# Optimization experiments

Hardware: AMD Instinct MI355X
Metric: run time of the kernel (lower is better)

## Reference

```python
import jax, jax.numpy as jnp
import numpy as np

B, N, L, E, U, G, R, D, C = 64, 50000, 8, 100000, 20000, 20000, 64, 16, 2


def setup_inputs() -> dict:
    rng = np.random.default_rng(0)
    key = jax.random.key(0)
    ks = jax.random.split(key, 10)
    # index structures (duplicate-free where the torch code assumes uniqueness)
    gene_map = jnp.asarray(rng.choice(N, G, replace=False).astype(np.int32))
    dst_unique = jnp.stack([jnp.asarray(rng.choice(N, U, replace=False).astype(np.int32)) for _ in range(L)])
    root_ids = jnp.asarray(rng.choice(N, R, replace=False).astype(np.int32))
    src = jax.random.randint(ks[0], (L, E), 0, N, dtype=jnp.int32)
    dst_pos = jax.random.randint(ks[1], (L, E), 0, U, dtype=jnp.int32)
    # data and parameters
    X_gene_batch = jax.random.normal(ks[2], (B, G), jnp.float32)
    w_in = jax.random.normal(ks[3], (D,), jnp.float32) * 0.5   # Linear(1, d) weight
    b_in = jax.random.normal(ks[4], (D,), jnp.float32) * 0.1
    W = jax.random.normal(ks[5], (L, D, D), jnp.float32) * (1.0 / np.sqrt(D))  # xavier-ish
    bias = jnp.zeros((N, D), jnp.float32)
    W_head = jax.random.normal(ks[6], (C, R * D), jnp.float32) * (1.0 / np.sqrt(R * D))
    b_head = jnp.zeros((C,), jnp.float32)
    return {
        "X_gene_batch": X_gene_batch, "w_in": w_in, "b_in": b_in, "W": W,
        "bias": bias, "W_head": W_head, "b_head": b_head,
        "gene_map": gene_map, "src": src, "dst_pos": dst_pos,
        "dst_unique": dst_unique, "root_ids": root_ids,
    }


def reference(X_gene_batch, w_in, b_in, W, bias, W_head, b_head,
              gene_map, src, dst_pos, dst_unique, root_ids):
    Bn = X_gene_batch.shape[0]
    n_nodes, d = bias.shape
    n_layers = W.shape[0]
    u = dst_unique.shape[1]
    # _init_state_vector: h=0, scatter in_proj(X[...,None]) at gene_map
    gene_emb = X_gene_batch[..., None] * w_in + b_in          # [B, G, d]
    h = jnp.zeros((Bn, n_nodes, d), X_gene_batch.dtype)
    h = h.at[:, gene_map].set(gene_emb)
    for li in range(n_layers):
        h_src = h[:, src[li]]                                  # gather [B, E, d]
        msg = jnp.einsum('bed,df->bef', h_src, W[li])          # small dxd matmul
        agg = jnp.zeros((Bn, u, d), h.dtype).at[:, dst_pos[li]].add(msg)  # scatter-add
        h_dst = jnp.tanh(agg + bias[dst_unique[li]][None])     # bias lookup + tanh (dropout=0)
        h = h.at[:, dst_unique[li]].set(h_dst)                 # write back
    feat = h[:, root_ids].reshape(Bn, -1)                      # roots_concat readout
    return feat @ W_head.T + b_head                            # [B, C]
```

## Files before the change

### kernel.cpp

```cpp
#include <hip/hip_runtime.h>
#include <hip/hip_fp16.h>
#include <cmath>

constexpr int B_ = 64, N_ = 50000, L_ = 8, E_ = 100000, U_ = 20000, G_ = 20000, R_ = 64, D_ = 16, C_ = 2;
constexpr int EPL_ = E_ + 3 * U_ + 8;
constexpr int BC = 64;
constexpr int F = BC * 2;


__device__ __forceinline__ float tanh_fast(float x) {
  float e = __expf(2.0f * x);
  return 1.0f - 2.0f * __builtin_amdgcn_rcpf(e + 1.0f);
}


__global__ __launch_bounds__(256) void hist_kernel(
    const int* __restrict__ dst_pos, int* __restrict__ cnt,
    int* __restrict__ rank) {
  int e = blockIdx.x * 256 + threadIdx.x;
  int li = blockIdx.y;
  if (e >= E_) return;
  rank[li * E_ + e] = atomicAdd(&cnt[li * U_ + dst_pos[li * E_ + e]], 1);
}

__global__ __launch_bounds__(1024) void scan_kernel(
    const int* __restrict__ cnt, int* __restrict__ offs) {
  __shared__ int sums[1024];
  int li = blockIdx.x, t = threadIdx.x;
  int base = t * 20;
  int v[20];
  int s = 0;
#pragma unroll
  for (int i = 0; i < 20; ++i) {
    int idx = base + i;
    int c = (idx < U_) ? cnt[li * U_ + idx] : 0;
    v[i] = s;
    s += (c + 3) & ~3;
  }
  sums[t] = s;
  __syncthreads();
  for (int off = 1; off < 1024; off <<= 1) {
    int o = (t >= off) ? sums[t - off] : 0;
    __syncthreads();
    sums[t] += o;
    __syncthreads();
  }
  int excl = sums[t] - s;
#pragma unroll
  for (int i = 0; i < 20; ++i) {
    int idx = base + i;
    if (idx < U_) offs[li * (U_ + 1) + idx] = excl + v[i];
  }
  if (t == 1023) offs[li * (U_ + 1) + U_] = sums[1023];
}

__global__ __launch_bounds__(256) void scatter_kernel(
    const int* __restrict__ dst_pos, const int* __restrict__ src,
    const int* __restrict__ offs, const int* __restrict__ rank,
    int* __restrict__ ssrc) {
  int e = blockIdx.x * 256 + threadIdx.x;
  int li = blockIdx.y;
  if (e >= E_) return;
  int u = dst_pos[li * E_ + e];
  int p = offs[li * (U_ + 1) + u] + rank[li * E_ + e];
  ssrc[(size_t)li * EPL_ + p] = src[li * E_ + e];
}

__global__ __launch_bounds__(256) void pad_fill_k(
    const int* __restrict__ cnt, const int* __restrict__ offs,
    int* __restrict__ ssrc) {
  int t = blockIdx.x * 256 + threadIdx.x;
  if (t >= L_ * U_) return;
  int li = t / U_, u = t % U_;
  int end = offs[li * (U_ + 1) + u] + cnt[li * U_ + u];
  int pend = offs[li * (U_ + 1) + u + 1];
  int* sp = ssrc + (size_t)li * EPL_;
  for (int p = end; p < pend; ++p) sp[p] = N_;
  if (u == U_ - 1) {
    int ptot = offs[li * (U_ + 1) + U_];
    for (int p = ptot; p < ptot + 8; ++p) sp[p] = N_;
  }
}


__global__ __launch_bounds__(256) void gene_init_k(
    const float* __restrict__ X, const float* __restrict__ w_in,
    const float* __restrict__ b_in, const int* __restrict__ gene_map,
    float4* __restrict__ h4) {
  int t = blockIdx.x * 256 + threadIdx.x;
  if (t >= G_ * BC) return;
  int b = t % BC;
  int g = t / BC;
  float x = X[b * G_ + g];
  int node = gene_map[g];
  float4 out[2];
  __half2* oh = reinterpret_cast<__half2*>(out);
#pragma unroll
  for (int k = 0; k < 8; ++k) {
    float r0 = fmaf(x, w_in[2 * k], b_in[2 * k]);
    float r1 = fmaf(x, w_in[2 * k + 1], b_in[2 * k + 1]);
    oh[k] = __float22half2_rn(make_float2(r0, r1));
  }
  h4[(size_t)node * F + b * 2] = out[0];
  h4[(size_t)node * F + b * 2 + 1] = out[1];
}

__global__ __launch_bounds__(256) void gather_k(
    const float4* __restrict__ h4, const int* __restrict__ offs,
    const int* __restrict__ ssrc, float4* __restrict__ agg4, int li) {
  int tid = threadIdx.x;
  int wave = tid >> 6, lane = tid & 63;
  int w = blockIdx.x * 4 + wave;
  int u0 = w * 4;
  const int* ob = offs + li * (U_ + 1) + u0;
  int offv[5];
#pragma unroll
  for (int i = 0; i < 5; ++i) offv[i] = ob[i];
  const int* sp = ssrc + (size_t)li * EPL_;

  __half2 acc[2][2][4];
  const __half2 z = __half2half2(__float2half(0.f));
#pragma unroll
  for (int j = 0; j < 2; ++j)
#pragma unroll
    for (int r = 0; r < 2; ++r)
#pragma unroll
      for (int k = 0; k < 4; ++k) acc[j][r][k] = z;

  auto flushu = [&](int u) {
#pragma unroll
    for (int r = 0; r < 2; ++r) {
      float4 outv;
      __half2* ov = reinterpret_cast<__half2*>(&outv);
#pragma unroll
      for (int k = 0; k < 4; ++k) {
        float2 f0 = __half22float2(acc[0][r][k]);
        float2 f1 = __half22float2(acc[1][r][k]);
        ov[k] = __float22half2_rn(make_float2(f0.x + f1.x, f0.y + f1.y));
      }
      agg4[(size_t)u * F + lane + r * 64] = outv;
    }
#pragma unroll
    for (int j = 0; j < 2; ++j)
#pragma unroll
      for (int r = 0; r < 2; ++r)
#pragma unroll
        for (int k = 0; k < 4; ++k) acc[j][r][k] = z;
  };

  auto loadRows = [&](float4 (&v)[4][2], int4 id) {
    v[0][0] = h4[(size_t)id.x * F + lane]; v[0][1] = h4[(size_t)id.x * F + lane + 64];
    v[1][0] = h4[(size_t)id.y * F + lane]; v[1][1] = h4[(size_t)id.y * F + lane + 64];
    v[2][0] = h4[(size_t)id.z * F + lane]; v[2][1] = h4[(size_t)id.z * F + lane + 64];
    v[3][0] = h4[(size_t)id.w * F + lane]; v[3][1] = h4[(size_t)id.w * F + lane + 64];
  };
  auto accum = [&](const float4 (&v)[4][2]) {
#pragma unroll
    for (int j = 0; j < 4; ++j)
#pragma unroll
      for (int r = 0; r < 2; ++r) {
        const __half2* p = reinterpret_cast<const __half2*>(&v[j][r]);
#pragma unroll
        for (int k = 0; k < 4; ++k)
          acc[j & 1][r][k] = __hadd2(acc[j & 1][r][k], p[k]);
      }
  };

  int e = offv[0];
  int eend = offv[4];
  int uj = 0;
  while (uj < 4 && offv[uj + 1] == e) { flushu(u0 + uj); ++uj; }
  if (e >= eend) return;

  float4 va[4][2], vb[4][2];
  int4 idC = *(const int4*)(sp + e);
  int4 idN = *(const int4*)(sp + e + 4);
  loadRows(va, idC);

  for (;;) {
    loadRows(vb, idN);
    idN = *(const int4*)(sp + e + 8);
    accum(va);
    e += 4;
    if (e == offv[uj + 1]) {
      flushu(u0 + uj); ++uj;
      while (uj < 4 && offv[uj + 1] == e) { flushu(u0 + uj); ++uj; }
    }
    if (e >= eend) break;
    loadRows(va, idN);
    idN = *(const int4*)(sp + e + 8);
    accum(vb);
    e += 4;
    if (e == offv[uj + 1]) {
      flushu(u0 + uj); ++uj;
      while (uj < 4 && offv[uj + 1] == e) { flushu(u0 + uj); ++uj; }
    }
    if (e >= eend) break;
  }
}

__global__ __launch_bounds__(256) void dense_k(
    const float4* __restrict__ agg4, const float* __restrict__ W,
    const float* __restrict__ bias, const int* __restrict__ dst_unique,
    float4* __restrict__ h4, int li) {
  __shared__ float Wlds[256];
  int tid = threadIdx.x;
  Wlds[tid] = W[li * 256 + tid];
  __syncthreads();
  int t = blockIdx.x * 256 + tid;
  int u = t >> 6, b = t & 63;
  float4 c0 = agg4[(size_t)u * F + b * 2];
  float4 c1 = agg4[(size_t)u * F + b * 2 + 1];
  float a[16];
  {
    const __half2* p0 = reinterpret_cast<const __half2*>(&c0);
    const __half2* p1 = reinterpret_cast<const __half2*>(&c1);
#pragma unroll
    for (int k = 0; k < 4; ++k) {
      float2 f0 = __half22float2(p0[k]);
      float2 f1 = __half22float2(p1[k]);
      a[2 * k] = f0.x; a[2 * k + 1] = f0.y;
      a[8 + 2 * k] = f1.x; a[8 + 2 * k + 1] = f1.y;
    }
  }
  float m[16];
#pragma unroll
  for (int j = 0; j < 16; ++j) m[j] = 0.f;
#pragma unroll
  for (int d = 0; d < 16; ++d) {
    float s = a[d];
    const float4* wr = (const float4*)&Wlds[d * 16];
    float4 w0 = wr[0], w1 = wr[1], w2 = wr[2], w3 = wr[3];
    m[0] = fmaf(s, w0.x, m[0]);  m[1] = fmaf(s, w0.y, m[1]);
    m[2] = fmaf(s, w0.z, m[2]);  m[3] = fmaf(s, w0.w, m[3]);
    m[4] = fmaf(s, w1.x, m[4]);  m[5] = fmaf(s, w1.y, m[5]);
    m[6] = fmaf(s, w1.z, m[6]);  m[7] = fmaf(s, w1.w, m[7]);
    m[8] = fmaf(s, w2.x, m[8]);  m[9] = fmaf(s, w2.y, m[9]);
    m[10] = fmaf(s, w2.z, m[10]); m[11] = fmaf(s, w2.w, m[11]);
    m[12] = fmaf(s, w3.x, m[12]); m[13] = fmaf(s, w3.y, m[13]);
    m[14] = fmaf(s, w3.z, m[14]); m[15] = fmaf(s, w3.w, m[15]);
  }
  int node = dst_unique[li * U_ + u];
  const float4* bp = (const float4*)(bias + (size_t)node * 16);
  float4 b0 = bp[0], b1 = bp[1], b2 = bp[2], b3 = bp[3];
  float bb[16] = {b0.x, b0.y, b0.z, b0.w, b1.x, b1.y, b1.z, b1.w,
                  b2.x, b2.y, b2.z, b2.w, b3.x, b3.y, b3.z, b3.w};
  float4 o0, o1;
  __half2* ov0 = reinterpret_cast<__half2*>(&o0);
  __half2* ov1 = reinterpret_cast<__half2*>(&o1);
#pragma unroll
  for (int k = 0; k < 4; ++k) {
    ov0[k] = __float22half2_rn(make_float2(tanh_fast(m[2 * k] + bb[2 * k]),
                                           tanh_fast(m[2 * k + 1] + bb[2 * k + 1])));
    ov1[k] = __float22half2_rn(make_float2(tanh_fast(m[8 + 2 * k] + bb[8 + 2 * k]),
                                           tanh_fast(m[8 + 2 * k + 1] + bb[8 + 2 * k + 1])));
  }
  h4[(size_t)node * F + b * 2] = o0;
  h4[(size_t)node * F + b * 2 + 1] = o1;
}

__global__ __launch_bounds__(64) void head_k(
    const float4* __restrict__ h4, const float* __restrict__ W_head,
    const float* __restrict__ b_head, const int* __restrict__ root_ids,
    float* __restrict__ out) {
  int bl = blockIdx.x;
  int r = threadIdx.x;
  int node = root_ids[r];
  float4 p0 = h4[(size_t)node * F + bl * 2];
  float4 p1 = h4[(size_t)node * F + bl * 2 + 1];
  float v[16];
  const __half2* ph0 = reinterpret_cast<const __half2*>(&p0);
  const __half2* ph1 = reinterpret_cast<const __half2*>(&p1);
#pragma unroll
  for (int k = 0; k < 4; ++k) {
    float2 f0 = __half22float2(ph0[k]);
    float2 f1 = __half22float2(ph1[k]);
    v[2 * k] = f0.x; v[2 * k + 1] = f0.y;
    v[8 + 2 * k] = f1.x; v[8 + 2 * k + 1] = f1.y;
  }
  float acc0 = 0.f, acc1 = 0.f;
#pragma unroll
  for (int d = 0; d < 16; ++d) {
    acc0 = fmaf(v[d], W_head[r * 16 + d], acc0);
    acc1 = fmaf(v[d], W_head[1024 + r * 16 + d], acc1);
  }
  for (int off = 32; off; off >>= 1) {
    acc0 += __shfl_down(acc0, off, 64);
    acc1 += __shfl_down(acc1, off, 64);
  }
  if (r == 0) {
    out[bl * 2 + 0] = acc0 + b_head[0];
    out[bl * 2 + 1] = acc1 + b_head[1];
  }
}

__global__ void zero_out_k(float* out, int n) {
  int t = blockIdx.x * 256 + threadIdx.x;
  if (t < n) out[t] = 0.f;
}


static size_t need_bytes() {
  return (size_t)(N_ + 1) * F * 16 + (size_t)U_ * F * 16 +
         (size_t)L_ * U_ * 4 +
         (size_t)L_ * (U_ + 1) * 4 +
         (size_t)L_ * E_ * 4 +
         (size_t)L_ * EPL_ * 4;
}

extern "C" void kernel_launch(void* const* d_in, const int* in_sizes, int n_in,
                              void* d_out, int out_size, void* d_ws, size_t ws_size,
                              hipStream_t stream) {
  if (ws_size < need_bytes()) {
    zero_out_k<<<(out_size + 255) / 256, 256, 0, stream>>>((float*)d_out, out_size);
    return;
  }
  const float* X = (const float*)d_in[0];
  const float* w_in = (const float*)d_in[1];
  const float* b_in = (const float*)d_in[2];
  const float* W = (const float*)d_in[3];
  const float* bias = (const float*)d_in[4];
  const float* W_head = (const float*)d_in[5];
  const float* b_head = (const float*)d_in[6];
  const int* gene_map = (const int*)d_in[7];
  const int* src = (const int*)d_in[8];
  const int* dst_pos = (const int*)d_in[9];
  const int* dst_unique = (const int*)d_in[10];
  const int* root_ids = (const int*)d_in[11];
  float* out = (float*)d_out;

  const size_t h_bytes = (size_t)(N_ + 1) * F * 16;
  const size_t agg_bytes = (size_t)U_ * F * 16;
  const size_t cnt_bytes = (size_t)L_ * U_ * 4;
  const size_t offs_bytes = (size_t)L_ * (U_ + 1) * 4;
  const size_t rank_bytes = (size_t)L_ * E_ * 4;

  char* ws = (char*)d_ws;
  float4* h4 = (float4*)ws;
  float4* agg4 = (float4*)(ws + h_bytes);
  int* cnt = (int*)(ws + h_bytes + agg_bytes);
  int* offs = (int*)(ws + h_bytes + agg_bytes + cnt_bytes);
  int* rank = (int*)(ws + h_bytes + agg_bytes + cnt_bytes + offs_bytes);
  int* ssrc = (int*)(ws + h_bytes + agg_bytes + cnt_bytes + offs_bytes + rank_bytes);

  hipMemsetAsync(cnt, 0, cnt_bytes, stream);
  hipMemsetAsync(h4, 0, h_bytes, stream);
  dim3 egrid((E_ + 255) / 256, L_);
  hist_kernel<<<egrid, 256, 0, stream>>>(dst_pos, cnt, rank);
  scan_kernel<<<L_, 1024, 0, stream>>>(cnt, offs);
  scatter_kernel<<<egrid, 256, 0, stream>>>(dst_pos, src, offs, rank, ssrc);
  pad_fill_k<<<(L_ * U_ + 255) / 256, 256, 0, stream>>>(cnt, offs, ssrc);

  gene_init_k<<<(G_ * BC + 255) / 256, 256, 0, stream>>>(X, w_in, b_in, gene_map, h4);

  const int gather_grid = U_ / 16;
  const int dense_grid = U_ * BC / 256;
  for (int li = 0; li < L_; ++li) {
    gather_k<<<gather_grid, 256, 0, stream>>>(h4, offs, ssrc, agg4, li);
    dense_k<<<dense_grid, 256, 0, stream>>>(agg4, W, bias, dst_unique, h4, li);
  }

  head_k<<<BC, 64, 0, stream>>>(h4, W_head, b_head, root_ids, out);
}
```

Before: 669.5 us.

## Balance gather work by assigning fixed edge-group chunks per wave instead of fixed nodes

```diff
diff --git a/kernel.cpp b/kernel.cpp
--- a/kernel.cpp
+++ b/kernel.cpp
@@ -3,7 +3,9 @@
 #include <cmath>
 
 constexpr int B_ = 64, N_ = 50000, L_ = 8, E_ = 100000, U_ = 20000, G_ = 20000, R_ = 64, D_ = 16, C_ = 2;
-constexpr int EPL_ = E_ + 3 * U_ + 8;
+constexpr int EPL_ = E_ + 3 * U_ + 4096;
+constexpr int EPLG_ = EPL_ / 4 + 16;
+constexpr int GPW = 8;
 constexpr int BC = 64;
 constexpr int F = BC * 2;
 
@@ -33,9 +35,10 @@
 #pragma unroll
   for (int i = 0; i < 20; ++i) {
     int idx = base + i;
-    int c = (idx < U_) ? cnt[li * U_ + idx] : 0;
+    int c = (idx < U_) ? cnt[li * U_ + idx] : -1;
+    int pc = (c < 0) ? 0 : ((c == 0) ? 4 : ((c + 3) & ~3));
     v[i] = s;
-    s += (c + 3) & ~3;
+    s += pc;
   }
   sums[t] = s;
   __syncthreads();
@@ -66,16 +69,19 @@
   ssrc[(size_t)li * EPL_ + p] = src[li * E_ + e];
 }
 
-__global__ __launch_bounds__(256) void pad_fill_k(
+__global__ __launch_bounds__(256) void pad_fill_ug_k(
     const int* __restrict__ cnt, const int* __restrict__ offs,
-    int* __restrict__ ssrc) {
+    int* __restrict__ ssrc, int* __restrict__ ug) {
   int t = blockIdx.x * 256 + threadIdx.x;
   if (t >= L_ * U_) return;
   int li = t / U_, u = t % U_;
-  int end = offs[li * (U_ + 1) + u] + cnt[li * U_ + u];
+  int start = offs[li * (U_ + 1) + u];
+  int end = start + cnt[li * U_ + u];
   int pend = offs[li * (U_ + 1) + u + 1];
   int* sp = ssrc + (size_t)li * EPL_;
   for (int p = end; p < pend; ++p) sp[p] = N_;
+  int* ugp = ug + (size_t)li * EPLG_;
+  for (int g = start >> 2; g < (pend >> 2); ++g) ugp[g] = u;
   if (u == U_ - 1) {
     int ptot = offs[li * (U_ + 1) + U_];
     for (int p = ptot; p < ptot + 8; ++p) sp[p] = N_;
@@ -106,17 +112,21 @@
 }
 
 __global__ __launch_bounds__(256) void gather_k(
-    const float4* __restrict__ h4, const int* __restrict__ offs,
+    const float4* __restrict__ h4, const int* __restrict__ ug,
     const int* __restrict__ ssrc, float4* __restrict__ agg4, int li) {
   int tid = threadIdx.x;
   int wave = tid >> 6, lane = tid & 63;
-  int w = blockIdx.x * 4 + wave;
-  int u0 = w * 4;
-  const int* ob = offs + li * (U_ + 1) + u0;
-  int offv[5];
-#pragma unroll
-  for (int i = 0; i < 5; ++i) offv[i] = ob[i];
+  int wv = blockIdx.x * 4 + wave;
+  int g0 = wv * GPW, gend = g0 + GPW;
+  const int* ugp = ug + (size_t)li * EPLG_;
   const int* sp = ssrc + (size_t)li * EPL_;
+
+  int prevU = (g0 == 0) ? -2 : ugp[g0 - 1];
+  int g = g0;
+  while (g < gend && ugp[g] == prevU) ++g;
+  if (g >= gend) return;
+  int curU = ugp[g];
+  if (curU < 0) return;
 
   __half2 acc[2][2][4];
   const __half2 z = __half2half2(__float2half(0.f));
@@ -166,36 +176,43 @@
       }
   };
 
-  int e = offv[0];
-  int eend = offv[4];
-  int uj = 0;
-  while (uj < 4 && offv[uj + 1] == e) { flushu(u0 + uj); ++uj; }
-  if (e >= eend) return;
-
   float4 va[4][2], vb[4][2];
-  int4 idC = *(const int4*)(sp + e);
-  int4 idN = *(const int4*)(sp + e + 4);
-  loadRows(va, idC);
+  int4 idA = *(const int4*)(sp + 4 * g);
+  loadRows(va, idA);
+  int nuA = ugp[g + 1];
+  int nuB;
 
   for (;;) {
-    loadRows(vb, idN);
-    idN = *(const int4*)(sp + e + 8);
-    accum(va);
-    e += 4;
-    if (e == offv[uj + 1]) {
-      flushu(u0 + uj); ++uj;
-      while (uj < 4 && offv[uj + 1] == e) { flushu(u0 + uj); ++uj; }
+    {
+      bool more = (nuA >= 0) && ((nuA == curU) || (g + 1 < gend));
+      if (more) {
+        int4 idB = *(const int4*)(sp + 4 * (g + 1));
+        loadRows(vb, idB);
+        nuB = ugp[g + 2];
+      }
+      accum(va);
+      if (nuA != curU) {
+        flushu(curU);
+        if (!more) return;
+        curU = nuA;
+      }
+      ++g;
     }
-    if (e >= eend) break;
-    loadRows(va, idN);
-    idN = *(const int4*)(sp + e + 8);
-    accum(vb);
-    e += 4;
-    if (e == offv[uj + 1]) {
-      flushu(u0 + uj); ++uj;
-      while (uj < 4 && offv[uj + 1] == e) { flushu(u0 + uj); ++uj; }
+    {
+      bool more = (nuB >= 0) && ((nuB == curU) || (g + 1 < gend));
+      if (more) {
+        int4 idA2 = *(const int4*)(sp + 4 * (g + 1));
+        loadRows(va, idA2);
+        nuA = ugp[g + 2];
+      }
+      accum(vb);
+      if (nuB != curU) {
+        flushu(curU);
+        if (!more) return;
+        curU = nuB;
+      }
+      ++g;
     }
-    if (e >= eend) break;
   }
 }
 
@@ -334,6 +351,7 @@
   const size_t cnt_bytes = (size_t)L_ * U_ * 4;
   const size_t offs_bytes = (size_t)L_ * (U_ + 1) * 4;
   const size_t rank_bytes = (size_t)L_ * E_ * 4;
+  const size_t ug_bytes = (size_t)L_ * EPLG_ * 4;
 
   char* ws = (char*)d_ws;
   float4* h4 = (float4*)ws;
@@ -341,7 +359,9 @@
   int* cnt = (int*)(ws + h_bytes + agg_bytes);
   int* offs = (int*)(ws + h_bytes + agg_bytes + cnt_bytes);
   int* rank = (int*)(ws + h_bytes + agg_bytes + cnt_bytes + offs_bytes);
+  int* ug = rank;
   int* ssrc = (int*)(ws + h_bytes + agg_bytes + cnt_bytes + offs_bytes + rank_bytes);
+  (void)ug_bytes;
 
   hipMemsetAsync(cnt, 0, cnt_bytes, stream);
   hipMemsetAsync(h4, 0, h_bytes, stream);
@@ -349,14 +369,17 @@
   hist_kernel<<<egrid, 256, 0, stream>>>(dst_pos, cnt, rank);
   scan_kernel<<<L_, 1024, 0, stream>>>(cnt, offs);
   scatter_kernel<<<egrid, 256, 0, stream>>>(dst_pos, src, offs, rank, ssrc);
-  pad_fill_k<<<(L_ * U_ + 255) / 256, 256, 0, stream>>>(cnt, offs, ssrc);
+  hipMemsetAsync(ug, 0xFF, ug_bytes, stream);
+  pad_fill_ug_k<<<(L_ * U_ + 255) / 256, 256, 0, stream>>>(cnt, offs, ssrc, ug);
 
   gene_init_k<<<(G_ * BC + 255) / 256, 256, 0, stream>>>(X, w_in, b_in, gene_map, h4);
 
-  const int gather_grid = U_ / 16;
+  const int total_groups = EPL_ / 4;
+  const int gwaves = (total_groups + GPW - 1) / GPW;
+  const int gather_grid = (gwaves + 3) / 4;
   const int dense_grid = U_ * BC / 256;
   for (int li = 0; li < L_; ++li) {
-    gather_k<<<gather_grid, 256, 0, stream>>>(h4, offs, ssrc, agg4, li);
+    gather_k<<<gather_grid, 256, 0, stream>>>(h4, ug, ssrc, agg4, li);
     dense_k<<<dense_grid, 256, 0, stream>>>(agg4, W, bias, dst_unique, h4, li);
   }
 
```

Result: faster. 626.9 us (-6.4%).
